# Performance work log

Hardware: AMD Instinct MI355X
Metric: run time of the kernel (lower is better)

Reference implementation:

```python
import jax, jax.numpy as jnp
import numpy as np

B, D_IN, H1, H2, LAT, K = 32768, 512, 256, 128, 64, 2048
BN_EPS = 1e-5
COMMIT = 0.25


def _linear_w(k, i, o):
    # xavier-uniform-ish init
    lim = np.sqrt(6.0 / (i + o)).astype(np.float32)
    return jax.random.uniform(k, (i, o), jnp.float32, -lim, lim)


def _bn_params(keys, n):
    g = jax.random.uniform(keys[0], (n,), jnp.float32, 0.5, 1.5)
    b = 0.1 * jax.random.normal(keys[1], (n,), jnp.float32)
    m = 0.1 * jax.random.normal(keys[2], (n,), jnp.float32)
    v = jax.random.uniform(keys[3], (n,), jnp.float32, 0.5, 1.5)
    return g, b, m, v


def setup_inputs() -> dict:
    key = jax.random.key(0)
    ks = jax.random.split(key, 32)
    inp = {"x": jax.random.normal(ks[0], (B, D_IN), jnp.float32)}
    # encoder: 512 -> 256 -> 128 -> 64
    inp["ew1"], inp["eb1"] = _linear_w(ks[1], D_IN, H1), jnp.zeros((H1,), jnp.float32)
    inp["eg1"], inp["ebt1"], inp["em1"], inp["ev1"] = _bn_params(jax.random.split(ks[2], 4), H1)
    inp["ew2"], inp["eb2"] = _linear_w(ks[3], H1, H2), jnp.zeros((H2,), jnp.float32)
    inp["eg2"], inp["ebt2"], inp["em2"], inp["ev2"] = _bn_params(jax.random.split(ks[4], 4), H2)
    inp["ew3"], inp["eb3"] = _linear_w(ks[5], H2, LAT), jnp.zeros((LAT,), jnp.float32)
    # codebook (num_embeddings, latent_dim)
    inp["codebook"] = _linear_w(ks[6], K, LAT).reshape(K, LAT)
    # decoder: 64 -> 128 -> 256 -> 512
    inp["dw1"], inp["db1"] = _linear_w(ks[7], LAT, H2), jnp.zeros((H2,), jnp.float32)
    inp["dg1"], inp["dbt1"], inp["dm1"], inp["dv1"] = _bn_params(jax.random.split(ks[8], 4), H2)
    inp["dw2"], inp["db2"] = _linear_w(ks[9], H2, H1), jnp.zeros((H1,), jnp.float32)
    inp["dg2"], inp["dbt2"], inp["dm2"], inp["dv2"] = _bn_params(jax.random.split(ks[10], 4), H1)
    inp["dw3"], inp["db3"] = _linear_w(ks[11], H1, D_IN), jnp.zeros((D_IN,), jnp.float32)
    return inp


def _bn(x, g, b, m, v):
    # BatchNorm1d in eval mode: running stats
    return (x - m) * (g * jax.lax.rsqrt(v + BN_EPS)) + b


def reference(x, ew1, eb1, eg1, ebt1, em1, ev1,
              ew2, eb2, eg2, ebt2, em2, ev2,
              ew3, eb3, codebook,
              dw1, db1, dg1, dbt1, dm1, dv1,
              dw2, db2, dg2, dbt2, dm2, dv2,
              dw3, db3):
    # ---- encoder MLP (Dropout is identity in eval) ----
    h = _bn(jax.nn.relu(x @ ew1 + eb1), eg1, ebt1, em1, ev1)
    h = _bn(jax.nn.relu(h @ ew2 + eb2), eg2, ebt2, em2, ev2)
    z_e = h @ ew3 + eb3  # [B, LAT]

    # ---- vector quantization: cdist + argmin + gather ----
    # squared L2 distance (argmin-equivalent to cdist p=2)
    d2 = (jnp.sum(z_e * z_e, axis=1, keepdims=True)
          + jnp.sum(codebook * codebook, axis=1)[None, :]
          - 2.0 * (z_e @ codebook.T))  # [B, K]
    idx = jnp.argmin(d2, axis=-1)  # [B]
    z_q = codebook[idx]  # gather, [B, LAT]

    codebook_loss = jnp.mean((z_q - jax.lax.stop_gradient(z_e)) ** 2)
    commit_loss = jnp.mean((z_e - jax.lax.stop_gradient(z_q)) ** 2)
    vq_loss = codebook_loss + COMMIT * commit_loss

    # straight-through estimator
    z_q = z_e + jax.lax.stop_gradient(z_q - z_e)

    # ---- decoder MLP ----
    h = _bn(jax.nn.relu(z_q @ dw1 + db1), dg1, dbt1, dm1, dv1)
    h = _bn(jax.nn.relu(h @ dw2 + db2), dg2, dbt2, dm2, dv2)
    x_recon = h @ dw3 + db3  # [B, D_IN]

    recon_err = jnp.mean((x_recon - x) ** 2)
    return x_recon, vq_loss, idx, recon_err
```

## Files before the change

### kernel.cpp

```cpp
#include <hip/hip_runtime.h>

#define B_ROWS 32768
#define D_IN   512
#define H1_N   256
#define H2_N   128
#define LAT_N  64
#define K_CB   2048

#define VQ_MARGIN 6.0e-3f
#define BK 32
#define BN 128

typedef __attribute__((ext_vector_type(8))) short s8v;
typedef __attribute__((ext_vector_type(4))) float f4v;

__device__ inline unsigned short f2bf(float f) {
    union { float f; unsigned u; } v; v.f = f;
    unsigned r = v.u + 0x7fffu + ((v.u >> 16) & 1u);
    return (unsigned short)(r >> 16);
}
__device__ inline float bf2f(unsigned short h) {
    union { unsigned u; float f; } v; v.u = ((unsigned)h) << 16;
    return v.f;
}

#define SWZ(row) ((((row) >> 2) & 7) << 3)

template <int MODE, int K, int CT, bool ASPLIT>
__global__ __launch_bounds__(256, 2) void mfma_gemm(
    const float* __restrict__ A_f32,
    const unsigned short* __restrict__ A_hi,
    const unsigned short* __restrict__ A_lo,
    const unsigned short* __restrict__ w_hi,
    const unsigned short* __restrict__ w_lo,
    const float* __restrict__ bias,
    const float* __restrict__ bn_g, const float* __restrict__ bn_b,
    const float* __restrict__ bn_m, const float* __restrict__ bn_v,
    unsigned short* __restrict__ out_hi, unsigned short* __restrict__ out_lo,
    float* __restrict__ out_f32,
    const float* __restrict__ xref, float* __restrict__ partials, int N)
{
    const int lane = threadIdx.x & 63;
    const int wv = threadIdx.x >> 6;
    const int wr = wv >> 1, wc = wv & 1;
    const int rbase = blockIdx.x * 128 + wr * 64;
    const int cbase = blockIdx.y * (32 * CT) + wc * (16 * CT);
    const int lr = lane & 15, lg = lane >> 4;

    f4v acc[4][CT];
#pragma unroll
    for (int rt = 0; rt < 4; ++rt)
#pragma unroll
        for (int ct = 0; ct < CT; ++ct)
            acc[rt][ct] = (f4v){0.f, 0.f, 0.f, 0.f};

    for (int ks = 0; ks < K / 32; ++ks) {
        s8v ah[4], al[4], bh[CT], bl[CT];
#pragma unroll
        for (int rt = 0; rt < 4; ++rt) {
            size_t off = (size_t)(rbase + rt * 16 + lr) * K + ks * 32 + lg * 8;
            if constexpr (ASPLIT) {
                const float* p = &A_f32[off];
                float4 v0 = *reinterpret_cast<const float4*>(p);
                float4 v1 = *reinterpret_cast<const float4*>(p + 4);
                float fv[8] = {v0.x, v0.y, v0.z, v0.w, v1.x, v1.y, v1.z, v1.w};
                unsigned uu[8], llv[8];
#pragma unroll
                for (int j = 0; j < 8; ++j) {
                    uu[j] = __float_as_uint(fv[j]);
                    float lo = fv[j] - __uint_as_float(uu[j] & 0xffff0000u);
                    llv[j] = __float_as_uint(lo);
                }
                union { s8v v; unsigned w[4]; } H, L;
#pragma unroll
                for (int m = 0; m < 4; ++m) {
                    H.w[m] = __builtin_amdgcn_perm(uu[2 * m + 1], uu[2 * m], 0x07060302u);
                    L.w[m] = __builtin_amdgcn_perm(llv[2 * m + 1], llv[2 * m], 0x07060302u);
                }
                ah[rt] = H.v;
                al[rt] = L.v;
            } else {
                ah[rt] = *reinterpret_cast<const s8v*>(&A_hi[off]);
                al[rt] = *reinterpret_cast<const s8v*>(&A_lo[off]);
            }
        }
#pragma unroll
        for (int ct = 0; ct < CT; ++ct) {
            size_t off = (size_t)(cbase + ct * 16 + lr) * K + ks * 32 + lg * 8;
            bh[ct] = *reinterpret_cast<const s8v*>(&w_hi[off]);
            bl[ct] = *reinterpret_cast<const s8v*>(&w_lo[off]);
        }
#pragma unroll
        for (int rt = 0; rt < 4; ++rt)
#pragma unroll
            for (int ct = 0; ct < CT; ++ct) {
                acc[rt][ct] = __builtin_amdgcn_mfma_f32_16x16x32_bf16(
                    ah[rt], bh[ct], acc[rt][ct], 0, 0, 0);
                acc[rt][ct] = __builtin_amdgcn_mfma_f32_16x16x32_bf16(
                    al[rt], bh[ct], acc[rt][ct], 0, 0, 0);
                acc[rt][ct] = __builtin_amdgcn_mfma_f32_16x16x32_bf16(
                    ah[rt], bl[ct], acc[rt][ct], 0, 0, 0);
            }
    }

    float sq = 0.f;
#pragma unroll
    for (int ct = 0; ct < CT; ++ct) {
        int col = cbase + ct * 16 + lr;
        float bi = bias[col];
        float sc = 0.f, sh = 0.f;
        if (MODE == 0) {
            float s = bn_g[col] * rsqrtf(bn_v[col] + 1e-5f);
            sc = s;
            sh = bn_b[col] - bn_m[col] * s;
        }
#pragma unroll
        for (int rt = 0; rt < 4; ++rt)
#pragma unroll
            for (int i = 0; i < 4; ++i) {
                int row = rbase + rt * 16 + lg * 4 + i;
                float v = acc[rt][ct][i] + bi;
                if (MODE == 0) v = fmaxf(v, 0.f) * sc + sh;
                if (MODE == 0 || MODE == 3) {
                    unsigned u = __float_as_uint(v);
                    out_hi[(size_t)row * N + col] = (unsigned short)(u >> 16);
                    out_lo[(size_t)row * N + col] =
                        f2bf(v - __uint_as_float(u & 0xffff0000u));
                }
                if (MODE == 2) {
                    float d = v - xref[(size_t)row * N + col];
                    sq = fmaf(d, d, sq);
                }
                if (MODE == 2 || MODE == 3)
                    out_f32[(size_t)row * N + col] = v;
            }
    }
    if (MODE == 2) {
        __shared__ float red[256];
        red[threadIdx.x] = sq;
        __syncthreads();
        for (int off = 128; off > 0; off >>= 1) {
            if (threadIdx.x < off) red[threadIdx.x] += red[threadIdx.x + off];
            __syncthreads();
        }
        if (threadIdx.x == 0)
            partials[blockIdx.y * gridDim.x + blockIdx.x] = red[0];
    }
}

template <int MODE, bool GATHER>
__global__ __launch_bounds__(256, 6) void rgemm(
    const int* __restrict__ rcnt, const int* __restrict__ rlist,
    const float* __restrict__ A, const float* __restrict__ W,
    const float* __restrict__ bias,
    const float* __restrict__ bn_g, const float* __restrict__ bn_b,
    const float* __restrict__ bn_m, const float* __restrict__ bn_v,
    float* __restrict__ out, int M, int N)
{
    const int count = min(rcnt[0], B_ROWS);
    const int row0 = blockIdx.x * 64;
    if (row0 >= count) return;
    __shared__ float sA[BK][64];
    __shared__ float sB[BK][BN];
    const int tid = threadIdx.x;
    const int tr = tid >> 4;
    const int tc = tid & 15;
    const int n0 = blockIdx.y * BN;

    float acc[4][8];
#pragma unroll
    for (int i = 0; i < 4; ++i)
#pragma unroll
        for (int j = 0; j < 8; ++j) acc[i][j] = 0.f;

    for (int k0 = 0; k0 < M; k0 += BK) {
#pragma unroll
        for (int it = 0; it < 2; ++it) {
            int s = tid + it * 256;
            int m = s >> 3;
            int kq = s & 7;
            int i = row0 + m;
            int src;
            if (GATHER) {
                int rr = (i < count) ? rlist[i] : 0;
                src = ((unsigned)rr < (unsigned)B_ROWS) ? rr : 0;
            } else {
                src = i;
            }
            float4 v = *reinterpret_cast<const float4*>(
                &A[(size_t)src * M + k0 + kq * 4]);
            int kk = kq * 4;
            sA[kk + 0][m ^ SWZ(kk + 0)] = v.x;
            sA[kk + 1][m ^ SWZ(kk + 1)] = v.y;
            sA[kk + 2][m ^ SWZ(kk + 2)] = v.z;
            sA[kk + 3][m ^ SWZ(kk + 3)] = v.w;
        }
#pragma unroll
        for (int it = 0; it < 4; ++it) {
            int s = tid + it * 256;
            int k = s >> 5;
            int nq = s & 31;
            int n = n0 + nq * 4;
            float4 v = make_float4(0.f, 0.f, 0.f, 0.f);
            if (n < N)
                v = *reinterpret_cast<const float4*>(&W[(size_t)(k0 + k) * N + n]);
            *reinterpret_cast<float4*>(&sB[k][nq * 4]) = v;
        }
        __syncthreads();
#pragma unroll 4
        for (int k = 0; k < BK; ++k) {
            int ac = (tr * 4) ^ SWZ(k);
            float4 a0 = *reinterpret_cast<float4*>(&sA[k][ac]);
            float a[4] = {a0.x, a0.y, a0.z, a0.w};
            float4 b0 = *reinterpret_cast<float4*>(&sB[k][tc * 4]);
            float4 b1 = *reinterpret_cast<float4*>(&sB[k][64 + tc * 4]);
            float b[8] = {b0.x, b0.y, b0.z, b0.w, b1.x, b1.y, b1.z, b1.w};
#pragma unroll
            for (int i = 0; i < 4; ++i)
#pragma unroll
                for (int j = 0; j < 8; ++j)
                    acc[i][j] = fmaf(a[i], b[j], acc[i][j]);
        }
        __syncthreads();
    }

    const int nb0 = n0 + tc * 4;
    const int nb1 = n0 + 64 + tc * 4;
    float bi[8], sc[8], sh[8];
#pragma unroll
    for (int g = 0; g < 2; ++g) {
        int nb = g ? nb1 : nb0;
        if (nb < N) {
#pragma unroll
            for (int j = 0; j < 4; ++j) {
                int n = nb + j;
                bi[g * 4 + j] = bias[n];
                if (MODE == 0) {
                    float s = bn_g[n] * rsqrtf(bn_v[n] + 1e-5f);
                    sc[g * 4 + j] = s;
                    sh[g * 4 + j] = bn_b[n] - bn_m[n] * s;
                }
            }
        }
    }
#pragma unroll
    for (int i = 0; i < 4; ++i) {
        int row = row0 + tr * 4 + i;
#pragma unroll
        for (int g = 0; g < 2; ++g) {
            int nb = g ? nb1 : nb0;
            if (nb < N) {
                float o[4];
#pragma unroll
                for (int j = 0; j < 4; ++j) {
                    float v = acc[i][g * 4 + j] + bi[g * 4 + j];
                    if (MODE == 0) {
                        v = v > 0.f ? v : 0.f;
                        v = v * sc[g * 4 + j] + sh[g * 4 + j];
                    }
                    o[j] = v;
                }
                *reinterpret_cast<float4*>(&out[(size_t)row * N + nb]) =
                    make_float4(o[0], o[1], o[2], o[3]);
            }
        }
    }
}

__device__ inline void wprep_body(const float* __restrict__ w,
                                  unsigned short* __restrict__ w_hi,
                                  unsigned short* __restrict__ w_lo,
                                  int K, int N, int idx)
{
    if (idx >= N * K) return;
    int n = idx / K, k = idx - n * K;
    float f = w[(size_t)k * N + n];
    unsigned u = __float_as_uint(f);
    float lo = f - __uint_as_float(u & 0xffff0000u);
    w_hi[idx] = (unsigned short)(u >> 16);
    w_lo[idx] = f2bf(lo);
}

__global__ __launch_bounds__(256) void prep_all(
    const float* __restrict__ dw3, unsigned short* w3hi, unsigned short* w3lo,
    const float* __restrict__ dw2, unsigned short* w2hi, unsigned short* w2lo,
    const float* __restrict__ dw1, unsigned short* w1hi, unsigned short* w1lo,
    const float* __restrict__ ew1, unsigned short* e1hi, unsigned short* e1lo,
    const float* __restrict__ ew2, unsigned short* e2hi, unsigned short* e2lo,
    const float* __restrict__ ew3, unsigned short* e3hi, unsigned short* e3lo,
    const float* __restrict__ cb, unsigned short* cb_hi, unsigned short* cb_lo,
    float* __restrict__ cn, int* __restrict__ rcnt, float* __restrict__ repairp)
{
    int bid = blockIdx.x;
    int tid = threadIdx.x;
    if (bid < 512) {
        wprep_body(dw3, w3hi, w3lo, H1_N, D_IN, bid * 256 + tid);
    } else if (bid < 640) {
        wprep_body(dw2, w2hi, w2lo, H2_N, H1_N, (bid - 512) * 256 + tid);
    } else if (bid < 672) {
        wprep_body(dw1, w1hi, w1lo, LAT_N, H2_N, (bid - 640) * 256 + tid);
    } else if (bid < 1184) {
        wprep_body(ew1, e1hi, e1lo, D_IN, H1_N, (bid - 672) * 256 + tid);
    } else if (bid < 1312) {
        wprep_body(ew2, e2hi, e2lo, H1_N, H2_N, (bid - 1184) * 256 + tid);
    } else if (bid < 1344) {
        wprep_body(ew3, e3hi, e3lo, H2_N, LAT_N, (bid - 1312) * 256 + tid);
    } else {
        int blk = bid - 1344;
        if (blk == 0) {
            if (tid == 0) rcnt[0] = 0;
            repairp[tid] = 0.f;
        }
        int j = blk * 256 + tid;
        float s = 0.f;
#pragma unroll
        for (int lq = 0; lq < 16; ++lq) {
            float4 v = *reinterpret_cast<const float4*>(&cb[(size_t)j * LAT_N + lq * 4]);
            float e[4] = {v.x, v.y, v.z, v.w};
            ushort4 h, l;
            unsigned short* hp = &h.x;
            unsigned short* lp = &l.x;
#pragma unroll
            for (int t = 0; t < 4; ++t) {
                s = fmaf(e[t], e[t], s);
                unsigned short hb = f2bf(e[t]);
                hp[t] = hb;
                lp[t] = f2bf(e[t] - bf2f(hb));
            }
            *reinterpret_cast<ushort4*>(&cb_hi[(size_t)j * LAT_N + lq * 4]) = h;
            *reinterpret_cast<ushort4*>(&cb_lo[(size_t)j * LAT_N + lq * 4]) = l;
        }
        cn[j] = s;
    }
}

__global__ __launch_bounds__(256) void vq_mfma(
    const unsigned short* __restrict__ zhi, const unsigned short* __restrict__ zlo,
    const unsigned short* __restrict__ cb_hi,
    const unsigned short* __restrict__ cb_lo, const float* __restrict__ cnorm,
    float4* __restrict__ cand)
{
    const int lane = threadIdx.x & 63;
    const int wid  = blockIdx.x * 4 + (threadIdx.x >> 6);
    const int rbase = (wid >> 3) * 64;
    const int cblk  = wid & 7;
    const int cbase = cblk * 256;
    const int lr = lane & 15;
    const int lg = lane >> 4;

    s8v a_hi[4][2], a_lo[4][2];
#pragma unroll
    for (int rt = 0; rt < 4; ++rt) {
        int row = rbase + rt * 16 + lr;
#pragma unroll
        for (int ks = 0; ks < 2; ++ks) {
            size_t off = (size_t)row * LAT_N + ks * 32 + lg * 8;
            a_hi[rt][ks] = *reinterpret_cast<const s8v*>(&zhi[off]);
            a_lo[rt][ks] = *reinterpret_cast<const s8v*>(&zlo[off]);
        }
    }

    float b1[4][4], b2[4][4];
    int j1[4][4];
#pragma unroll
    for (int rt = 0; rt < 4; ++rt)
#pragma unroll
        for (int i = 0; i < 4; ++i) {
            b1[rt][i] = 3.4e38f; b2[rt][i] = 3.4e38f; j1[rt][i] = 0;
        }

    for (int ct = 0; ct < 16; ++ct) {
        int col = cbase + ct * 16 + lr;
        const unsigned short* ph = &cb_hi[(size_t)col * LAT_N + lg * 8];
        const unsigned short* pl = &cb_lo[(size_t)col * LAT_N + lg * 8];
        s8v bh0 = *reinterpret_cast<const s8v*>(ph);
        s8v bh1 = *reinterpret_cast<const s8v*>(ph + 32);
        s8v bl0 = *reinterpret_cast<const s8v*>(pl);
        s8v bl1 = *reinterpret_cast<const s8v*>(pl + 32);
        float cn = cnorm[col];
#pragma unroll
        for (int rt = 0; rt < 4; ++rt) {
            f4v acc = {0.f, 0.f, 0.f, 0.f};
            acc = __builtin_amdgcn_mfma_f32_16x16x32_bf16(a_hi[rt][0], bh0, acc, 0, 0, 0);
            acc = __builtin_amdgcn_mfma_f32_16x16x32_bf16(a_hi[rt][1], bh1, acc, 0, 0, 0);
            acc = __builtin_amdgcn_mfma_f32_16x16x32_bf16(a_lo[rt][0], bh0, acc, 0, 0, 0);
            acc = __builtin_amdgcn_mfma_f32_16x16x32_bf16(a_lo[rt][1], bh1, acc, 0, 0, 0);
            acc = __builtin_amdgcn_mfma_f32_16x16x32_bf16(a_hi[rt][0], bl0, acc, 0, 0, 0);
            acc = __builtin_amdgcn_mfma_f32_16x16x32_bf16(a_hi[rt][1], bl1, acc, 0, 0, 0);
#pragma unroll
            for (int i = 0; i < 4; ++i) {
                float d = fmaf(-2.f, acc[i], cn);
                if (d < b1[rt][i]) {
                    b2[rt][i] = b1[rt][i];
                    b1[rt][i] = d;
                    j1[rt][i] = col;
                } else if (d < b2[rt][i]) {
                    b2[rt][i] = d;
                }
            }
        }
    }

#pragma unroll
    for (int off = 1; off < 16; off <<= 1) {
#pragma unroll
        for (int rt = 0; rt < 4; ++rt)
#pragma unroll
            for (int i = 0; i < 4; ++i) {
                float o1 = __shfl_xor(b1[rt][i], off);
                float o2 = __shfl_xor(b2[rt][i], off);
                int oj = __shfl_xor(j1[rt][i], off);
                float nb2 = fminf(fmaxf(b1[rt][i], o1), fminf(b2[rt][i], o2));
                if (o1 < b1[rt][i] ||
                    (o1 == b1[rt][i] && oj < j1[rt][i])) {
                    b1[rt][i] = o1;
                    j1[rt][i] = oj;
                }
                b2[rt][i] = nb2;
            }
    }
    if (lr == 0) {
#pragma unroll
        for (int rt = 0; rt < 4; ++rt)
#pragma unroll
            for (int i = 0; i < 4; ++i) {
                int row = rbase + rt * 16 + lg * 4 + i;
                cand[(size_t)row * 8 + cblk] = make_float4(
                    b1[rt][i], __int_as_float(j1[rt][i]), b2[rt][i], 0.f);
            }
    }
}

__global__ __launch_bounds__(256) void vq_merge(
    const float4* __restrict__ cand, const float* __restrict__ z,
    const float* __restrict__ cb,
    const unsigned short* __restrict__ cbhi,
    const unsigned short* __restrict__ cblo,
    unsigned short* __restrict__ zqhi, unsigned short* __restrict__ zqlo,
    float* __restrict__ idxf,
    int* __restrict__ rlist, int* __restrict__ rcnt,
    float* __restrict__ mergep)
{
    __shared__ float red[256];
    int tid = threadIdx.x;
    int row = blockIdx.x * 256 + tid;
    const float4* c = &cand[(size_t)row * 8];
    float4 c0 = c[0];
    float b1 = c0.x, b2 = c0.z;
    int j1 = __float_as_int(c0.y);
#pragma unroll
    for (int t = 1; t < 8; ++t) {
        float4 ct = c[t];
        float o1 = ct.x, o2 = ct.z;
        int oj = __float_as_int(ct.y);
        float nb2 = fminf(fmaxf(b1, o1), fminf(b2, o2));
        if (o1 < b1 || (o1 == b1 && oj < j1)) { b1 = o1; j1 = oj; }
        b2 = nb2;
    }
    idxf[row] = (float)j1;
    float sq = 0.f;
    if (b2 - b1 >= VQ_MARGIN) {
#pragma unroll
        for (int lq = 0; lq < 16; ++lq) {
            float4 cv = *reinterpret_cast<const float4*>(&cb[(size_t)j1 * LAT_N + lq * 4]);
            float4 zv = *reinterpret_cast<const float4*>(&z[(size_t)row * LAT_N + lq * 4]);
            float d0 = cv.x - zv.x, d1 = cv.y - zv.y;
            float d2 = cv.z - zv.z, d3 = cv.w - zv.w;
            sq = fmaf(d0, d0, sq); sq = fmaf(d1, d1, sq);
            sq = fmaf(d2, d2, sq); sq = fmaf(d3, d3, sq);
        }
        const uint4* gh = reinterpret_cast<const uint4*>(&cbhi[(size_t)j1 * LAT_N]);
        const uint4* gl = reinterpret_cast<const uint4*>(&cblo[(size_t)j1 * LAT_N]);
        uint4* dh = reinterpret_cast<uint4*>(&zqhi[(size_t)row * LAT_N]);
        uint4* dl = reinterpret_cast<uint4*>(&zqlo[(size_t)row * LAT_N]);
#pragma unroll
        for (int q = 0; q < 8; ++q) { dh[q] = gh[q]; dl[q] = gl[q]; }
    } else {
        int s = atomicAdd(rcnt, 1);
        if (s < B_ROWS) rlist[s] = row;
    }
    red[tid] = sq;
    __syncthreads();
    for (int off = 128; off > 0; off >>= 1) {
        if (tid < off) red[tid] += red[tid + off];
        __syncthreads();
    }
    if (tid == 0) mergep[blockIdx.x] = red[0];
}

#define RB 8
__global__ __launch_bounds__(256) void repair_scan(
    const int* __restrict__ rcnt, const int* __restrict__ rlist,
    const float* __restrict__ zr,
    const float* __restrict__ cb, const float* __restrict__ cn,
    const unsigned short* __restrict__ cbhi,
    const unsigned short* __restrict__ cblo,
    unsigned short* __restrict__ zqhi, unsigned short* __restrict__ zqlo,
    float* __restrict__ idxf, float* __restrict__ repairp)
{
    __shared__ float sz[RB][LAT_N];
    __shared__ float rv[256];
    __shared__ int ri[256];
    const int tid = threadIdx.x;
    const int count = min(rcnt[0], B_ROWS);
    if (blockIdx.x * RB >= count) return;
    float lsum = 0.f;
    for (int base = blockIdx.x * RB; base < count; base += gridDim.x * RB) {
        int nr = min(RB, count - base);
        __syncthreads();
        for (int s = tid; s < nr * LAT_N; s += 256) {
            int r = s >> 6, d = s & 63;
            sz[r][d] = zr[(size_t)(base + r) * LAT_N + d];
        }
        __syncthreads();
        float bv[RB];
        int bj[RB];
#pragma unroll
        for (int r = 0; r < RB; ++r) { bv[r] = 3.4e38f; bj[r] = 0; }
        for (int k = 0; k < K_CB / 256; ++k) {
            int cidx = tid + k * 256;
            float a[RB];
#pragma unroll
            for (int r = 0; r < RB; ++r) a[r] = 0.f;
            const float* cp = &cb[(size_t)cidx * LAT_N];
#pragma unroll 2
            for (int d4 = 0; d4 < 16; ++d4) {
                float4 cv = *reinterpret_cast<const float4*>(cp + d4 * 4);
#pragma unroll
                for (int r = 0; r < RB; ++r) {
                    a[r] = fmaf(sz[r][d4 * 4 + 0], cv.x, a[r]);
                    a[r] = fmaf(sz[r][d4 * 4 + 1], cv.y, a[r]);
                    a[r] = fmaf(sz[r][d4 * 4 + 2], cv.z, a[r]);
                    a[r] = fmaf(sz[r][d4 * 4 + 3], cv.w, a[r]);
                }
            }
            float cnv = cn[cidx];
#pragma unroll
            for (int r = 0; r < RB; ++r) {
                float d = fmaf(-2.f, a[r], cnv);
                if (d < bv[r] || (d == bv[r] && cidx < bj[r])) {
                    bv[r] = d; bj[r] = cidx;
                }
            }
        }
        for (int r = 0; r < RB; ++r) {
            if (r >= nr) break;
            rv[tid] = bv[r];
            ri[tid] = bj[r];
            __syncthreads();
            for (int off = 128; off > 0; off >>= 1) {
                if (tid < off) {
                    float ov = rv[tid + off];
                    int oi = ri[tid + off];
                    if (ov < rv[tid] || (ov == rv[tid] && oi < ri[tid])) {
                        rv[tid] = ov; ri[tid] = oi;
                    }
                }
                __syncthreads();
            }
            int bjf = ri[0];
            int rr = rlist[base + r];
            bool ok = (unsigned)rr < (unsigned)B_ROWS;
            rr = ok ? rr : 0;
            if (tid == 0 && ok) idxf[rr] = (float)bjf;
            float v = 0.f;
            if (tid < 64) {
                float d = cb[(size_t)bjf * LAT_N + tid] - sz[r][tid];
                v = d * d;
            }
            __syncthreads();
            rv[tid] = v;
            __syncthreads();
            for (int off = 128; off > 0; off >>= 1) {
                if (tid < off) rv[tid] += rv[tid + off];
                __syncthreads();
            }
            if (tid == 0) lsum += rv[0];
            if (ok) {
                if (tid < 8)
                    reinterpret_cast<uint4*>(&zqhi[(size_t)rr * LAT_N])[tid] =
                        reinterpret_cast<const uint4*>(&cbhi[(size_t)bjf * LAT_N])[tid];
                else if (tid < 16)
                    reinterpret_cast<uint4*>(&zqlo[(size_t)rr * LAT_N])[tid - 8] =
                        reinterpret_cast<const uint4*>(&cblo[(size_t)bjf * LAT_N])[tid - 8];
            }
            __syncthreads();
        }
    }
    if (tid == 0) repairp[blockIdx.x] = lsum;
}

__global__ __launch_bounds__(256) void finalize_kernel(
    const float* __restrict__ mergep, int nm,
    const float* __restrict__ repairp, int nr,
    const float* __restrict__ rep, int nre,
    float* __restrict__ vq_out, float* __restrict__ re_out)
{
    __shared__ float s[256];
    int tid = threadIdx.x;
    float a = 0.f;
    for (int i = tid; i < nm; i += 256) a += mergep[i];
    for (int i = tid; i < nr; i += 256) a += repairp[i];
    s[tid] = a;
    __syncthreads();
    for (int off = 128; off > 0; off >>= 1) {
        if (tid < off) s[tid] += s[tid + off];
        __syncthreads();
    }
    if (tid == 0) *vq_out = 1.25f * s[0] / (float)(B_ROWS * LAT_N);
    __syncthreads();
    float b = 0.f;
    for (int i = tid; i < nre; i += 256) b += rep[i];
    s[tid] = b;
    __syncthreads();
    for (int off = 128; off > 0; off >>= 1) {
        if (tid < off) s[tid] += s[tid + off];
        __syncthreads();
    }
    if (tid == 0) *re_out = s[0] / (float)(B_ROWS * D_IN);
}

extern "C" void kernel_launch(void* const* d_in, const int* in_sizes, int n_in,
                              void* d_out, int out_size, void* d_ws, size_t ws_size,
                              hipStream_t stream)
{
    const float* x    = (const float*)d_in[0];
    const float* ew1  = (const float*)d_in[1];
    const float* eb1  = (const float*)d_in[2];
    const float* eg1  = (const float*)d_in[3];
    const float* ebt1 = (const float*)d_in[4];
    const float* em1  = (const float*)d_in[5];
    const float* ev1  = (const float*)d_in[6];
    const float* ew2  = (const float*)d_in[7];
    const float* eb2  = (const float*)d_in[8];
    const float* eg2  = (const float*)d_in[9];
    const float* ebt2 = (const float*)d_in[10];
    const float* em2  = (const float*)d_in[11];
    const float* ev2  = (const float*)d_in[12];
    const float* ew3  = (const float*)d_in[13];
    const float* eb3  = (const float*)d_in[14];
    const float* cb   = (const float*)d_in[15];
    const float* dw1  = (const float*)d_in[16];
    const float* db1  = (const float*)d_in[17];
    const float* dg1  = (const float*)d_in[18];
    const float* dbt1 = (const float*)d_in[19];
    const float* dm1  = (const float*)d_in[20];
    const float* dv1  = (const float*)d_in[21];
    const float* dw2  = (const float*)d_in[22];
    const float* db2  = (const float*)d_in[23];
    const float* dg2  = (const float*)d_in[24];
    const float* dbt2 = (const float*)d_in[25];
    const float* dm2  = (const float*)d_in[26];
    const float* dv2  = (const float*)d_in[27];
    const float* dw3  = (const float*)d_in[28];
    const float* db3  = (const float*)d_in[29];

    float* outf = (float*)d_out;
    const size_t XR_OFF = 0;
    const size_t VQ_OFF = (size_t)B_ROWS * D_IN;
    const size_t IDX_OFF = VQ_OFF + 1;
    const size_t RE_OFF = IDX_OFF + B_ROWS;

    float* wsf = (float*)d_ws;
    size_t off = 0;
    float* buf256 = wsf + off; off += (size_t)B_ROWS * H1_N;
    float* buf128 = wsf + off; off += (size_t)B_ROWS * H2_N;
    float* zbuf   = wsf + off; off += (size_t)B_ROWS * LAT_N;
    float* zr     = wsf + off; off += (size_t)B_ROWS * LAT_N;
    float* cnbuf  = wsf + off; off += K_CB;
    float* mergep = wsf + off; off += 128;
    float* repairp= wsf + off; off += 256;
    float* rep    = wsf + off; off += 1024;
    unsigned short* cbhi = (unsigned short*)(wsf + off); off += K_CB * LAT_N / 2;
    unsigned short* cblo = (unsigned short*)(wsf + off); off += K_CB * LAT_N / 2;
    float4* candb = (float4*)(wsf + off); off += (size_t)B_ROWS * 8 * 4;
    int* rcnt  = (int*)(wsf + off); off += 16;
    int* rlist = (int*)(wsf + off); off += B_ROWS;
    unsigned short* w1hi = (unsigned short*)(wsf + off); off += (H2_N * LAT_N) / 2;
    unsigned short* w1lo = (unsigned short*)(wsf + off); off += (H2_N * LAT_N) / 2;
    unsigned short* w2hi = (unsigned short*)(wsf + off); off += (H1_N * H2_N) / 2;
    unsigned short* w2lo = (unsigned short*)(wsf + off); off += (H1_N * H2_N) / 2;
    unsigned short* w3hi = (unsigned short*)(wsf + off); off += (D_IN * H1_N) / 2;
    unsigned short* w3lo = (unsigned short*)(wsf + off); off += (D_IN * H1_N) / 2;
    unsigned short* e1hi = (unsigned short*)(wsf + off); off += (D_IN * H1_N) / 2;
    unsigned short* e1lo = (unsigned short*)(wsf + off); off += (D_IN * H1_N) / 2;
    unsigned short* e2hi = (unsigned short*)(wsf + off); off += (H1_N * H2_N) / 2;
    unsigned short* e2lo = (unsigned short*)(wsf + off); off += (H1_N * H2_N) / 2;
    unsigned short* e3hi = (unsigned short*)(wsf + off); off += (H2_N * LAT_N) / 2;
    unsigned short* e3lo = (unsigned short*)(wsf + off); off += (H2_N * LAT_N) / 2;
    unsigned short* zqhi = (unsigned short*)(wsf + off); off += (size_t)B_ROWS * LAT_N / 2;
    unsigned short* zqlo = (unsigned short*)(wsf + off); off += (size_t)B_ROWS * LAT_N / 2;

    unsigned short* eh1hi = (unsigned short*)buf256;
    unsigned short* eh1lo = (unsigned short*)(buf256 + (size_t)B_ROWS * 128);
    unsigned short* zhi   = (unsigned short*)buf256;
    unsigned short* zlo   = (unsigned short*)(buf256 + (size_t)B_ROWS * 32);
    float*          h1r   = buf256;
    unsigned short* dh2hi = (unsigned short*)buf256;
    unsigned short* dh2lo = (unsigned short*)(buf256 + (size_t)B_ROWS * 128);
    unsigned short* eh2hi = (unsigned short*)buf128;
    unsigned short* eh2lo = (unsigned short*)(buf128 + (size_t)B_ROWS * 64);
    float*          h2r   = buf128;
    unsigned short* dh1hi = (unsigned short*)buf128;
    unsigned short* dh1lo = (unsigned short*)(buf128 + (size_t)B_ROWS * 64);

    dim3 blk(256);
    const int GXM = B_ROWS / 128;

    prep_all<<<dim3(1352), blk, 0, stream>>>(
        dw3, w3hi, w3lo, dw2, w2hi, w2lo, dw1, w1hi, w1lo,
        ew1, e1hi, e1lo, ew2, e2hi, e2lo, ew3, e3hi, e3lo,
        cb, cbhi, cblo, cnbuf, rcnt, repairp);

    mfma_gemm<0, D_IN, 4, true><<<dim3(GXM, H1_N / 128), blk, 0, stream>>>(
        x, nullptr, nullptr, e1hi, e1lo, eb1, eg1, ebt1, em1, ev1,
        eh1hi, eh1lo, nullptr, nullptr, nullptr, H1_N);
    mfma_gemm<0, H1_N, 4, false><<<dim3(GXM, 1), blk, 0, stream>>>(
        nullptr, eh1hi, eh1lo, e2hi, e2lo, eb2, eg2, ebt2, em2, ev2,
        eh2hi, eh2lo, nullptr, nullptr, nullptr, H2_N);
    mfma_gemm<3, H2_N, 2, false><<<dim3(GXM, 1), blk, 0, stream>>>(
        nullptr, eh2hi, eh2lo, e3hi, e3lo, eb3, nullptr, nullptr, nullptr, nullptr,
        zhi, zlo, zbuf, nullptr, nullptr, LAT_N);

    vq_mfma<<<dim3(1024), blk, 0, stream>>>(zhi, zlo, cbhi, cblo, cnbuf, candb);
    vq_merge<<<dim3(B_ROWS / 256), blk, 0, stream>>>(
        candb, zbuf, cb, cbhi, cblo, zqhi, zqlo,
        outf + IDX_OFF, rlist, rcnt, mergep);

    rgemm<0, true><<<dim3(B_ROWS / 64, 2), blk, 0, stream>>>(
        rcnt, rlist, x, ew1, eb1, eg1, ebt1, em1, ev1, h1r, D_IN, H1_N);
    rgemm<0, false><<<dim3(B_ROWS / 64, 1), blk, 0, stream>>>(
        rcnt, rlist, h1r, ew2, eb2, eg2, ebt2, em2, ev2, h2r, H1_N, H2_N);
    rgemm<1, false><<<dim3(B_ROWS / 64, 1), blk, 0, stream>>>(
        rcnt, rlist, h2r, ew3, eb3, nullptr, nullptr, nullptr, nullptr,
        zr, H2_N, LAT_N);
    repair_scan<<<dim3(256), blk, 0, stream>>>(
        rcnt, rlist, zr, cb, cnbuf, cbhi, cblo, zqhi, zqlo,
        outf + IDX_OFF, repairp);

    mfma_gemm<0, LAT_N, 4, false><<<dim3(GXM, 1), blk, 0, stream>>>(
        nullptr, zqhi, zqlo, w1hi, w1lo, db1, dg1, dbt1, dm1, dv1,
        dh1hi, dh1lo, nullptr, nullptr, nullptr, H2_N);
    mfma_gemm<0, H2_N, 4, false><<<dim3(GXM, H1_N / 128), blk, 0, stream>>>(
        nullptr, dh1hi, dh1lo, w2hi, w2lo, db2, dg2, dbt2, dm2, dv2,
        dh2hi, dh2lo, nullptr, nullptr, nullptr, H1_N);
    mfma_gemm<2, H1_N, 4, false><<<dim3(GXM, D_IN / 128), blk, 0, stream>>>(
        nullptr, dh2hi, dh2lo, w3hi, w3lo, db3, nullptr, nullptr, nullptr, nullptr,
        nullptr, nullptr, outf + XR_OFF, x, rep, D_IN);

    finalize_kernel<<<dim3(1), blk, 0, stream>>>(
        mergep, 128, repairp, 256, rep, 1024, outf + VQ_OFF, outf + RE_OFF);
}
```

Measured before the change: 479.3 us.

## Double-buffer MFMA GEMM operand loads and shrink row tiles for occupancy

The GEMM kernel now prefetches the next k-step's A and B fragments into a second register set while MFMAs run on the current set, hiding global-load latency. The row tile per block is halved (RT template parameter), which doubles the grid size, and launch bounds are raised to allow 3-4 blocks per CU. The partials buffer for the reconstruction error grows to match the larger grid. In exchange the double buffers raise register pressure, and smaller tiles reduce weight reuse per block.

```diff
diff --git a/kernel.cpp b/kernel.cpp
--- a/kernel.cpp
+++ b/kernel.cpp
@@ -26,8 +26,8 @@
 
 #define SWZ(row) ((((row) >> 2) & 7) << 3)
 
-template <int MODE, int K, int CT, bool ASPLIT>
-__global__ __launch_bounds__(256, 2) void mfma_gemm(
+template <int MODE, int K, int RT, int CT, bool ASPLIT>
+__global__ __launch_bounds__(256, (CT >= 4) ? 3 : 4) void mfma_gemm(
     const float* __restrict__ A_f32,
     const unsigned short* __restrict__ A_hi,
     const unsigned short* __restrict__ A_lo,
@@ -40,68 +40,104 @@
     float* __restrict__ out_f32,
     const float* __restrict__ xref, float* __restrict__ partials, int N)
 {
+    constexpr int NK = K / 32;
     const int lane = threadIdx.x & 63;
     const int wv = threadIdx.x >> 6;
     const int wr = wv >> 1, wc = wv & 1;
-    const int rbase = blockIdx.x * 128 + wr * 64;
-    const int cbase = blockIdx.y * (32 * CT) + wc * (16 * CT);
+    const int rbase = blockIdx.x * (RT * 32) + wr * (RT * 16);
+    const int cbase = blockIdx.y * (CT * 32) + wc * (CT * 16);
     const int lr = lane & 15, lg = lane >> 4;
 
-    f4v acc[4][CT];
-#pragma unroll
-    for (int rt = 0; rt < 4; ++rt)
+    f4v acc[RT][CT];
+#pragma unroll
+    for (int rt = 0; rt < RT; ++rt)
 #pragma unroll
         for (int ct = 0; ct < CT; ++ct)
             acc[rt][ct] = (f4v){0.f, 0.f, 0.f, 0.f};
 
-    for (int ks = 0; ks < K / 32; ++ks) {
-        s8v ah[4], al[4], bh[CT], bl[CT];
-#pragma unroll
-        for (int rt = 0; rt < 4; ++rt) {
-            size_t off = (size_t)(rbase + rt * 16 + lr) * K + ks * 32 + lg * 8;
-            if constexpr (ASPLIT) {
-                const float* p = &A_f32[off];
-                float4 v0 = *reinterpret_cast<const float4*>(p);
-                float4 v1 = *reinterpret_cast<const float4*>(p + 4);
-                float fv[8] = {v0.x, v0.y, v0.z, v0.w, v1.x, v1.y, v1.z, v1.w};
-                unsigned uu[8], llv[8];
-#pragma unroll
-                for (int j = 0; j < 8; ++j) {
-                    uu[j] = __float_as_uint(fv[j]);
-                    float lo = fv[j] - __uint_as_float(uu[j] & 0xffff0000u);
-                    llv[j] = __float_as_uint(lo);
-                }
-                union { s8v v; unsigned w[4]; } H, L;
-#pragma unroll
-                for (int m = 0; m < 4; ++m) {
-                    H.w[m] = __builtin_amdgcn_perm(uu[2 * m + 1], uu[2 * m], 0x07060302u);
-                    L.w[m] = __builtin_amdgcn_perm(llv[2 * m + 1], llv[2 * m], 0x07060302u);
-                }
-                ah[rt] = H.v;
-                al[rt] = L.v;
-            } else {
-                ah[rt] = *reinterpret_cast<const s8v*>(&A_hi[off]);
-                al[rt] = *reinterpret_cast<const s8v*>(&A_lo[off]);
-            }
-        }
-#pragma unroll
-        for (int ct = 0; ct < CT; ++ct) {
-            size_t off = (size_t)(cbase + ct * 16 + lr) * K + ks * 32 + lg * 8;
-            bh[ct] = *reinterpret_cast<const s8v*>(&w_hi[off]);
-            bl[ct] = *reinterpret_cast<const s8v*>(&w_lo[off]);
-        }
-#pragma unroll
-        for (int rt = 0; rt < 4; ++rt)
-#pragma unroll
-            for (int ct = 0; ct < CT; ++ct) {
-                acc[rt][ct] = __builtin_amdgcn_mfma_f32_16x16x32_bf16(
-                    ah[rt], bh[ct], acc[rt][ct], 0, 0, 0);
-                acc[rt][ct] = __builtin_amdgcn_mfma_f32_16x16x32_bf16(
-                    al[rt], bh[ct], acc[rt][ct], 0, 0, 0);
-                acc[rt][ct] = __builtin_amdgcn_mfma_f32_16x16x32_bf16(
-                    ah[rt], bl[ct], acc[rt][ct], 0, 0, 0);
-            }
-    }
+    s8v ahA[RT], alA[RT], bhA[CT], blA[CT];
+    s8v ahB[RT], alB[RT], bhB[CT], blB[CT];
+    float4 rwA[RT][2], rwB[RT][2];
+
+#define LOAD_A(S, KS)                                                         \
+    {                                                                         \
+        _Pragma("unroll")                                                     \
+        for (int rt = 0; rt < RT; ++rt) {                                     \
+            size_t aoff = (size_t)(rbase + rt * 16 + lr) * K + (KS) * 32 + lg * 8; \
+            if constexpr (ASPLIT) {                                           \
+                rw##S[rt][0] = *reinterpret_cast<const float4*>(&A_f32[aoff]);      \
+                rw##S[rt][1] = *reinterpret_cast<const float4*>(&A_f32[aoff + 4]);  \
+            } else {                                                          \
+                ah##S[rt] = *reinterpret_cast<const s8v*>(&A_hi[aoff]);       \
+                al##S[rt] = *reinterpret_cast<const s8v*>(&A_lo[aoff]);       \
+            }                                                                 \
+        }                                                                     \
+    }
+
+#define LOAD_B(S, KS)                                                         \
+    {                                                                         \
+        _Pragma("unroll")                                                     \
+        for (int ct = 0; ct < CT; ++ct) {                                     \
+            size_t woff = (size_t)(cbase + ct * 16 + lr) * K + (KS) * 32 + lg * 8; \
+            bh##S[ct] = *reinterpret_cast<const s8v*>(&w_hi[woff]);           \
+            bl##S[ct] = *reinterpret_cast<const s8v*>(&w_lo[woff]);           \
+        }                                                                     \
+    }
+
+#define CONVERT(S)                                                            \
+    if constexpr (ASPLIT) {                                                   \
+        _Pragma("unroll")                                                     \
+        for (int rt = 0; rt < RT; ++rt) {                                     \
+            float fv[8] = {rw##S[rt][0].x, rw##S[rt][0].y, rw##S[rt][0].z,    \
+                           rw##S[rt][0].w, rw##S[rt][1].x, rw##S[rt][1].y,    \
+                           rw##S[rt][1].z, rw##S[rt][1].w};                   \
+            unsigned uu[8], llv[8];                                           \
+            _Pragma("unroll")                                                 \
+            for (int j = 0; j < 8; ++j) {                                     \
+                uu[j] = __float_as_uint(fv[j]);                               \
+                float lo = fv[j] - __uint_as_float(uu[j] & 0xffff0000u);      \
+                llv[j] = __float_as_uint(lo);                                 \
+            }                                                                 \
+            union { s8v v; unsigned w[4]; } Hh, Ll;                           \
+            _Pragma("unroll")                                                 \
+            for (int m = 0; m < 4; ++m) {                                     \
+                Hh.w[m] = __builtin_amdgcn_perm(uu[2 * m + 1], uu[2 * m], 0x07060302u);   \
+                Ll.w[m] = __builtin_amdgcn_perm(llv[2 * m + 1], llv[2 * m], 0x07060302u); \
+            }                                                                 \
+            ah##S[rt] = Hh.v;                                                 \
+            al##S[rt] = Ll.v;                                                 \
+        }                                                                     \
+    }
+
+#define MFMA_STEP(S)                                                          \
+    {                                                                         \
+        _Pragma("unroll")                                                     \
+        for (int rt = 0; rt < RT; ++rt)                                       \
+            _Pragma("unroll")                                                 \
+            for (int ct = 0; ct < CT; ++ct) {                                 \
+                acc[rt][ct] = __builtin_amdgcn_mfma_f32_16x16x32_bf16(        \
+                    ah##S[rt], bh##S[ct], acc[rt][ct], 0, 0, 0);              \
+                acc[rt][ct] = __builtin_amdgcn_mfma_f32_16x16x32_bf16(        \
+                    al##S[rt], bh##S[ct], acc[rt][ct], 0, 0, 0);              \
+                acc[rt][ct] = __builtin_amdgcn_mfma_f32_16x16x32_bf16(        \
+                    ah##S[rt], bl##S[ct], acc[rt][ct], 0, 0, 0);              \
+            }                                                                 \
+    }
+
+    LOAD_A(A, 0); LOAD_B(A, 0); CONVERT(A);
+#pragma unroll
+    for (int k2 = 0; k2 < NK / 2; ++k2) {
+        LOAD_A(B, 2 * k2 + 1); LOAD_B(B, 2 * k2 + 1);
+        MFMA_STEP(A);
+        CONVERT(B);
+        if (k2 + 1 < NK / 2) { LOAD_A(A, 2 * k2 + 2); LOAD_B(A, 2 * k2 + 2); }
+        MFMA_STEP(B);
+        if (k2 + 1 < NK / 2) CONVERT(A);
+    }
+#undef LOAD_A
+#undef LOAD_B
+#undef CONVERT
+#undef MFMA_STEP
 
     float sq = 0.f;
 #pragma unroll
@@ -115,7 +151,7 @@
             sh = bn_b[col] - bn_m[col] * s;
         }
 #pragma unroll
-        for (int rt = 0; rt < 4; ++rt)
+        for (int rt = 0; rt < RT; ++rt)
 #pragma unroll
             for (int i = 0; i < 4; ++i) {
                 int row = rbase + rt * 16 + lg * 4 + i;
@@ -670,7 +706,7 @@
     float* cnbuf  = wsf + off; off += K_CB;
     float* mergep = wsf + off; off += 128;
     float* repairp= wsf + off; off += 256;
-    float* rep    = wsf + off; off += 1024;
+    float* rep    = wsf + off; off += 2048;
     unsigned short* cbhi = (unsigned short*)(wsf + off); off += K_CB * LAT_N / 2;
     unsigned short* cblo = (unsigned short*)(wsf + off); off += K_CB * LAT_N / 2;
     float4* candb = (float4*)(wsf + off); off += (size_t)B_ROWS * 8 * 4;
@@ -705,20 +741,20 @@
     unsigned short* dh1lo = (unsigned short*)(buf128 + (size_t)B_ROWS * 64);
 
     dim3 blk(256);
-    const int GXM = B_ROWS / 128;
+    const int GM64 = B_ROWS / 64;
 
     prep_all<<<dim3(1352), blk, 0, stream>>>(
         dw3, w3hi, w3lo, dw2, w2hi, w2lo, dw1, w1hi, w1lo,
         ew1, e1hi, e1lo, ew2, e2hi, e2lo, ew3, e3hi, e3lo,
         cb, cbhi, cblo, cnbuf, rcnt, repairp);
 
-    mfma_gemm<0, D_IN, 4, true><<<dim3(GXM, H1_N / 128), blk, 0, stream>>>(
+    mfma_gemm<0, D_IN, 2, 4, true><<<dim3(GM64, H1_N / 128), blk, 0, stream>>>(
         x, nullptr, nullptr, e1hi, e1lo, eb1, eg1, ebt1, em1, ev1,
         eh1hi, eh1lo, nullptr, nullptr, nullptr, H1_N);
-    mfma_gemm<0, H1_N, 4, false><<<dim3(GXM, 1), blk, 0, stream>>>(
+    mfma_gemm<0, H1_N, 2, 2, false><<<dim3(GM64, H2_N / 64), blk, 0, stream>>>(
         nullptr, eh1hi, eh1lo, e2hi, e2lo, eb2, eg2, ebt2, em2, ev2,
         eh2hi, eh2lo, nullptr, nullptr, nullptr, H2_N);
-    mfma_gemm<3, H2_N, 2, false><<<dim3(GXM, 1), blk, 0, stream>>>(
+    mfma_gemm<3, H2_N, 2, 2, false><<<dim3(GM64, 1), blk, 0, stream>>>(
         nullptr, eh2hi, eh2lo, e3hi, e3lo, eb3, nullptr, nullptr, nullptr, nullptr,
         zhi, zlo, zbuf, nullptr, nullptr, LAT_N);
 
@@ -727,27 +763,27 @@
         candb, zbuf, cb, cbhi, cblo, zqhi, zqlo,
         outf + IDX_OFF, rlist, rcnt, mergep);
 
-    rgemm<0, true><<<dim3(B_ROWS / 64, 2), blk, 0, stream>>>(
+    rgemm<0, true><<<dim3(GM64, 2), blk, 0, stream>>>(
         rcnt, rlist, x, ew1, eb1, eg1, ebt1, em1, ev1, h1r, D_IN, H1_N);
-    rgemm<0, false><<<dim3(B_ROWS / 64, 1), blk, 0, stream>>>(
+    rgemm<0, false><<<dim3(GM64, 1), blk, 0, stream>>>(
         rcnt, rlist, h1r, ew2, eb2, eg2, ebt2, em2, ev2, h2r, H1_N, H2_N);
-    rgemm<1, false><<<dim3(B_ROWS / 64, 1), blk, 0, stream>>>(
+    rgemm<1, false><<<dim3(GM64, 1), blk, 0, stream>>>(
         rcnt, rlist, h2r, ew3, eb3, nullptr, nullptr, nullptr, nullptr,
         zr, H2_N, LAT_N);
     repair_scan<<<dim3(256), blk, 0, stream>>>(
         rcnt, rlist, zr, cb, cnbuf, cbhi, cblo, zqhi, zqlo,
         outf + IDX_OFF, repairp);
 
-    mfma_gemm<0, LAT_N, 4, false><<<dim3(GXM, 1), blk, 0, stream>>>(
+    mfma_gemm<0, LAT_N, 2, 2, false><<<dim3(GM64, H2_N / 64), blk, 0, stream>>>(
         nullptr, zqhi, zqlo, w1hi, w1lo, db1, dg1, dbt1, dm1, dv1,
         dh1hi, dh1lo, nullptr, nullptr, nullptr, H2_N);
-    mfma_gemm<0, H2_N, 4, false><<<dim3(GXM, H1_N / 128), blk, 0, stream>>>(
+    mfma_gemm<0, H2_N, 2, 4, false><<<dim3(GM64, H1_N / 128), blk, 0, stream>>>(
         nullptr, dh1hi, dh1lo, w2hi, w2lo, db2, dg2, dbt2, dm2, dv2,
         dh2hi, dh2lo, nullptr, nullptr, nullptr, H1_N);
-    mfma_gemm<2, H1_N, 4, false><<<dim3(GXM, D_IN / 128), blk, 0, stream>>>(
+    mfma_gemm<2, H1_N, 2, 4, false><<<dim3(GM64, D_IN / 128), blk, 0, stream>>>(
         nullptr, dh2hi, dh2lo, w3hi, w3lo, db3, nullptr, nullptr, nullptr, nullptr,
         nullptr, nullptr, outf + XR_OFF, x, rep, D_IN);
 
     finalize_kernel<<<dim3(1), blk, 0, stream>>>(
-        mergep, 128, repairp, 256, rep, 1024, outf + VQ_OFF, outf + RE_OFF);
-}
+        mergep, 128, repairp, 256, rep, 2048, outf + VQ_OFF, outf + RE_OFF);
+}
```

Result: slower. 531.9 us (+11.0%).

## Store bf16 hi/lo operands in MFMA-fragment-packed tiled layout

Applied to the files above, without the earlier changes.

Introduces a packed tile layout (16 rows x 32 k per 512-element block) for all bf16 hi/lo activations, weights and codebook, so each wave's fragment loads become contiguous 16-byte reads across lanes instead of strided row accesses. GEMM epilogues, weight prep, VQ gather and repair copy are rewritten to write and read this layout. Weight prep now packs 8 k values per thread with vector stores, which cuts the prep grid size. Epilogue stores stay scalar 2-byte writes at scattered packed addresses, which may cost store efficiency.

```diff
diff --git a/kernel.cpp b/kernel.cpp
--- a/kernel.cpp
+++ b/kernel.cpp
@@ -22,6 +22,11 @@
 __device__ inline float bf2f(unsigned short h) {
     union { unsigned u; float f; } v; v.u = ((unsigned)h) << 16;
     return v.f;
+}
+
+__device__ inline int pidx(int r, int k, int K) {
+    return ((r >> 4) * (K >> 5) + (k >> 5)) * 512 + (((k >> 3) & 3) << 7)
+         + ((r & 15) << 3) + (k & 7);
 }
 
 #define SWZ(row) ((((row) >> 2) & 7) << 3)
@@ -58,9 +63,9 @@
         s8v ah[4], al[4], bh[CT], bl[CT];
 #pragma unroll
         for (int rt = 0; rt < 4; ++rt) {
-            size_t off = (size_t)(rbase + rt * 16 + lr) * K + ks * 32 + lg * 8;
             if constexpr (ASPLIT) {
-                const float* p = &A_f32[off];
+                size_t aoff = (size_t)(rbase + rt * 16 + lr) * K + ks * 32 + lg * 8;
+                const float* p = &A_f32[aoff];
                 float4 v0 = *reinterpret_cast<const float4*>(p);
                 float4 v1 = *reinterpret_cast<const float4*>(p + 4);
                 float fv[8] = {v0.x, v0.y, v0.z, v0.w, v1.x, v1.y, v1.z, v1.w};
@@ -80,13 +85,14 @@
                 ah[rt] = H.v;
                 al[rt] = L.v;
             } else {
+                int off = (((rbase >> 4) + rt) * (K >> 5) + ks) * 512 + lg * 128 + lr * 8;
                 ah[rt] = *reinterpret_cast<const s8v*>(&A_hi[off]);
                 al[rt] = *reinterpret_cast<const s8v*>(&A_lo[off]);
             }
         }
 #pragma unroll
         for (int ct = 0; ct < CT; ++ct) {
-            size_t off = (size_t)(cbase + ct * 16 + lr) * K + ks * 32 + lg * 8;
+            int off = (((cbase >> 4) + ct) * (K >> 5) + ks) * 512 + lg * 128 + lr * 8;
             bh[ct] = *reinterpret_cast<const s8v*>(&w_hi[off]);
             bl[ct] = *reinterpret_cast<const s8v*>(&w_lo[off]);
         }
@@ -123,9 +129,9 @@
                 if (MODE == 0) v = fmaxf(v, 0.f) * sc + sh;
                 if (MODE == 0 || MODE == 3) {
                     unsigned u = __float_as_uint(v);
-                    out_hi[(size_t)row * N + col] = (unsigned short)(u >> 16);
-                    out_lo[(size_t)row * N + col] =
-                        f2bf(v - __uint_as_float(u & 0xffff0000u));
+                    int p = pidx(row, col, N);
+                    out_hi[p] = (unsigned short)(u >> 16);
+                    out_lo[p] = f2bf(v - __uint_as_float(u & 0xffff0000u));
                 }
                 if (MODE == 2) {
                     float d = v - xref[(size_t)row * N + col];
@@ -267,18 +273,26 @@
     }
 }
 
-__device__ inline void wprep_body(const float* __restrict__ w,
-                                  unsigned short* __restrict__ w_hi,
-                                  unsigned short* __restrict__ w_lo,
-                                  int K, int N, int idx)
-{
-    if (idx >= N * K) return;
-    int n = idx / K, k = idx - n * K;
-    float f = w[(size_t)k * N + n];
-    unsigned u = __float_as_uint(f);
-    float lo = f - __uint_as_float(u & 0xffff0000u);
-    w_hi[idx] = (unsigned short)(u >> 16);
-    w_lo[idx] = f2bf(lo);
+__device__ inline void wprep_packed(const float* __restrict__ w,
+                                    unsigned short* __restrict__ w_hi,
+                                    unsigned short* __restrict__ w_lo,
+                                    int K, int N, int t)
+{
+    if (t >= N * (K >> 3)) return;
+    int n = t / (K >> 3);
+    int k0 = (t - n * (K >> 3)) << 3;
+    union { unsigned short s[8]; uint4 v; } H, L;
+#pragma unroll
+    for (int j = 0; j < 8; ++j) {
+        float f = w[(size_t)(k0 + j) * N + n];
+        unsigned u = __float_as_uint(f);
+        float lo = f - __uint_as_float(u & 0xffff0000u);
+        H.s[j] = (unsigned short)(u >> 16);
+        L.s[j] = f2bf(lo);
+    }
+    int p = pidx(n, k0, K);
+    *reinterpret_cast<uint4*>(&w_hi[p]) = H.v;
+    *reinterpret_cast<uint4*>(&w_lo[p]) = L.v;
 }
 
 __global__ __launch_bounds__(256) void prep_all(
@@ -293,20 +307,20 @@
 {
     int bid = blockIdx.x;
     int tid = threadIdx.x;
-    if (bid < 512) {
-        wprep_body(dw3, w3hi, w3lo, H1_N, D_IN, bid * 256 + tid);
-    } else if (bid < 640) {
-        wprep_body(dw2, w2hi, w2lo, H2_N, H1_N, (bid - 512) * 256 + tid);
-    } else if (bid < 672) {
-        wprep_body(dw1, w1hi, w1lo, LAT_N, H2_N, (bid - 640) * 256 + tid);
-    } else if (bid < 1184) {
-        wprep_body(ew1, e1hi, e1lo, D_IN, H1_N, (bid - 672) * 256 + tid);
-    } else if (bid < 1312) {
-        wprep_body(ew2, e2hi, e2lo, H1_N, H2_N, (bid - 1184) * 256 + tid);
-    } else if (bid < 1344) {
-        wprep_body(ew3, e3hi, e3lo, H2_N, LAT_N, (bid - 1312) * 256 + tid);
+    if (bid < 64) {
+        wprep_packed(dw3, w3hi, w3lo, H1_N, D_IN, bid * 256 + tid);
+    } else if (bid < 80) {
+        wprep_packed(dw2, w2hi, w2lo, H2_N, H1_N, (bid - 64) * 256 + tid);
+    } else if (bid < 84) {
+        wprep_packed(dw1, w1hi, w1lo, LAT_N, H2_N, (bid - 80) * 256 + tid);
+    } else if (bid < 148) {
+        wprep_packed(ew1, e1hi, e1lo, D_IN, H1_N, (bid - 84) * 256 + tid);
+    } else if (bid < 164) {
+        wprep_packed(ew2, e2hi, e2lo, H1_N, H2_N, (bid - 148) * 256 + tid);
+    } else if (bid < 168) {
+        wprep_packed(ew3, e3hi, e3lo, H2_N, LAT_N, (bid - 164) * 256 + tid);
     } else {
-        int blk = bid - 1344;
+        int blk = bid - 168;
         if (blk == 0) {
             if (tid == 0) rcnt[0] = 0;
             repairp[tid] = 0.f;
@@ -314,21 +328,21 @@
         int j = blk * 256 + tid;
         float s = 0.f;
 #pragma unroll
-        for (int lq = 0; lq < 16; ++lq) {
-            float4 v = *reinterpret_cast<const float4*>(&cb[(size_t)j * LAT_N + lq * 4]);
-            float e[4] = {v.x, v.y, v.z, v.w};
-            ushort4 h, l;
-            unsigned short* hp = &h.x;
-            unsigned short* lp = &l.x;
-#pragma unroll
-            for (int t = 0; t < 4; ++t) {
+        for (int g = 0; g < 8; ++g) {
+            float4 v0 = *reinterpret_cast<const float4*>(&cb[(size_t)j * LAT_N + g * 8]);
+            float4 v1 = *reinterpret_cast<const float4*>(&cb[(size_t)j * LAT_N + g * 8 + 4]);
+            float e[8] = {v0.x, v0.y, v0.z, v0.w, v1.x, v1.y, v1.z, v1.w};
+            union { unsigned short us[8]; uint4 v; } H, L;
+#pragma unroll
+            for (int t = 0; t < 8; ++t) {
                 s = fmaf(e[t], e[t], s);
                 unsigned short hb = f2bf(e[t]);
-                hp[t] = hb;
-                lp[t] = f2bf(e[t] - bf2f(hb));
-            }
-            *reinterpret_cast<ushort4*>(&cb_hi[(size_t)j * LAT_N + lq * 4]) = h;
-            *reinterpret_cast<ushort4*>(&cb_lo[(size_t)j * LAT_N + lq * 4]) = l;
+                H.us[t] = hb;
+                L.us[t] = f2bf(e[t] - bf2f(hb));
+            }
+            int p = pidx(j, g * 8, LAT_N);
+            *reinterpret_cast<uint4*>(&cb_hi[p]) = H.v;
+            *reinterpret_cast<uint4*>(&cb_lo[p]) = L.v;
         }
         cn[j] = s;
     }
@@ -351,10 +365,9 @@
     s8v a_hi[4][2], a_lo[4][2];
 #pragma unroll
     for (int rt = 0; rt < 4; ++rt) {
-        int row = rbase + rt * 16 + lr;
 #pragma unroll
         for (int ks = 0; ks < 2; ++ks) {
-            size_t off = (size_t)row * LAT_N + ks * 32 + lg * 8;
+            int off = (((rbase >> 4) + rt) * 2 + ks) * 512 + lg * 128 + lr * 8;
             a_hi[rt][ks] = *reinterpret_cast<const s8v*>(&zhi[off]);
             a_lo[rt][ks] = *reinterpret_cast<const s8v*>(&zlo[off]);
         }
@@ -371,12 +384,12 @@
 
     for (int ct = 0; ct < 16; ++ct) {
         int col = cbase + ct * 16 + lr;
-        const unsigned short* ph = &cb_hi[(size_t)col * LAT_N + lg * 8];
-        const unsigned short* pl = &cb_lo[(size_t)col * LAT_N + lg * 8];
-        s8v bh0 = *reinterpret_cast<const s8v*>(ph);
-        s8v bh1 = *reinterpret_cast<const s8v*>(ph + 32);
-        s8v bl0 = *reinterpret_cast<const s8v*>(pl);
-        s8v bl1 = *reinterpret_cast<const s8v*>(pl + 32);
+        int t0 = (((cbase >> 4) + ct) * 2 + 0) * 512 + lg * 128 + lr * 8;
+        int t1 = t0 + 512;
+        s8v bh0 = *reinterpret_cast<const s8v*>(&cb_hi[t0]);
+        s8v bh1 = *reinterpret_cast<const s8v*>(&cb_hi[t1]);
+        s8v bl0 = *reinterpret_cast<const s8v*>(&cb_lo[t0]);
+        s8v bl1 = *reinterpret_cast<const s8v*>(&cb_lo[t1]);
         float cn = cnorm[col];
 #pragma unroll
         for (int rt = 0; rt < 4; ++rt) {
@@ -469,12 +482,15 @@
             sq = fmaf(d0, d0, sq); sq = fmaf(d1, d1, sq);
             sq = fmaf(d2, d2, sq); sq = fmaf(d3, d3, sq);
         }
-        const uint4* gh = reinterpret_cast<const uint4*>(&cbhi[(size_t)j1 * LAT_N]);
-        const uint4* gl = reinterpret_cast<const uint4*>(&cblo[(size_t)j1 * LAT_N]);
-        uint4* dh = reinterpret_cast<uint4*>(&zqhi[(size_t)row * LAT_N]);
-        uint4* dl = reinterpret_cast<uint4*>(&zqlo[(size_t)row * LAT_N]);
-#pragma unroll
-        for (int q = 0; q < 8; ++q) { dh[q] = gh[q]; dl[q] = gl[q]; }
+#pragma unroll
+        for (int g = 0; g < 8; ++g) {
+            int sp = pidx(j1, g * 8, LAT_N);
+            int dp = pidx(row, g * 8, LAT_N);
+            *reinterpret_cast<uint4*>(&zqhi[dp]) =
+                *reinterpret_cast<const uint4*>(&cbhi[sp]);
+            *reinterpret_cast<uint4*>(&zqlo[dp]) =
+                *reinterpret_cast<const uint4*>(&cblo[sp]);
+        }
     } else {
         int s = atomicAdd(rcnt, 1);
         if (s < B_ROWS) rlist[s] = row;
@@ -577,12 +593,15 @@
             }
             if (tid == 0) lsum += rv[0];
             if (ok) {
-                if (tid < 8)
-                    reinterpret_cast<uint4*>(&zqhi[(size_t)rr * LAT_N])[tid] =
-                        reinterpret_cast<const uint4*>(&cbhi[(size_t)bjf * LAT_N])[tid];
-                else if (tid < 16)
-                    reinterpret_cast<uint4*>(&zqlo[(size_t)rr * LAT_N])[tid - 8] =
-                        reinterpret_cast<const uint4*>(&cblo[(size_t)bjf * LAT_N])[tid - 8];
+                if (tid < 8) {
+                    int g = tid;
+                    *reinterpret_cast<uint4*>(&zqhi[pidx(rr, g * 8, LAT_N)]) =
+                        *reinterpret_cast<const uint4*>(&cbhi[pidx(bjf, g * 8, LAT_N)]);
+                } else if (tid < 16) {
+                    int g = tid - 8;
+                    *reinterpret_cast<uint4*>(&zqlo[pidx(rr, g * 8, LAT_N)]) =
+                        *reinterpret_cast<const uint4*>(&cblo[pidx(bjf, g * 8, LAT_N)]);
+                }
             }
             __syncthreads();
         }
@@ -706,8 +725,9 @@
 
     dim3 blk(256);
     const int GXM = B_ROWS / 128;
-
-    prep_all<<<dim3(1352), blk, 0, stream>>>(
+    const int GM64 = B_ROWS / 64;
+
+    prep_all<<<dim3(176), blk, 0, stream>>>(
         dw3, w3hi, w3lo, dw2, w2hi, w2lo, dw1, w1hi, w1lo,
         ew1, e1hi, e1lo, ew2, e2hi, e2lo, ew3, e3hi, e3lo,
         cb, cbhi, cblo, cnbuf, rcnt, repairp);
@@ -727,11 +747,11 @@
         candb, zbuf, cb, cbhi, cblo, zqhi, zqlo,
         outf + IDX_OFF, rlist, rcnt, mergep);
 
-    rgemm<0, true><<<dim3(B_ROWS / 64, 2), blk, 0, stream>>>(
+    rgemm<0, true><<<dim3(GM64, 2), blk, 0, stream>>>(
         rcnt, rlist, x, ew1, eb1, eg1, ebt1, em1, ev1, h1r, D_IN, H1_N);
-    rgemm<0, false><<<dim3(B_ROWS / 64, 1), blk, 0, stream>>>(
+    rgemm<0, false><<<dim3(GM64, 1), blk, 0, stream>>>(
         rcnt, rlist, h1r, ew2, eb2, eg2, ebt2, em2, ev2, h2r, H1_N, H2_N);
-    rgemm<1, false><<<dim3(B_ROWS / 64, 1), blk, 0, stream>>>(
+    rgemm<1, false><<<dim3(GM64, 1), blk, 0, stream>>>(
         rcnt, rlist, h2r, ew3, eb3, nullptr, nullptr, nullptr, nullptr,
         zr, H2_N, LAT_N);
     repair_scan<<<dim3(256), blk, 0, stream>>>(
```

After: 434.7 us. 1.1x faster.
